# Performance work log

Measured on AMD Instinct MI355X. Metric: run time of the kernel, lower is better.

The kernel has to match this reference:

```python
import jax, jax.numpy as jnp
import numpy as np
import math

B, T, D, H = 2, 2048, 1024, 16
DH = D // H


def setup_inputs() -> dict:
    key = jax.random.key(0)
    k1, k2, k3 = jax.random.split(key, 3)
    scale_in = 1.0 / math.sqrt(D)
    x = jax.random.normal(k1, (B, T, D), dtype=jnp.float32)
    w_qkv = jax.random.normal(k2, (D, 3 * D), dtype=jnp.float32) * scale_in
    b_qkv = jnp.zeros((3 * D,), dtype=jnp.float32)
    w_out = jax.random.normal(k3, (D, D), dtype=jnp.float32) * scale_in
    b_out = jnp.zeros((D,), dtype=jnp.float32)
    return {"x": x, "w_qkv": w_qkv, "b_qkv": b_qkv, "w_out": w_out, "b_out": b_out}


def reference(x, w_qkv, b_qkv, w_out, b_out):
    # Fused QKV projection: [B,T,3D]
    qkv = x @ w_qkv + b_qkv
    q, k, v = jnp.split(qkv, 3, axis=-1)
    # [B,H,T,DH]
    q = q.reshape(B, T, H, DH).transpose(0, 2, 1, 3)
    k = k.reshape(B, T, H, DH).transpose(0, 2, 1, 3)
    v = v.reshape(B, T, H, DH).transpose(0, 2, 1, 3)
    # scores: [B,H,T,T]
    scores = jnp.einsum('bhqd,bhkd->bhqk', q, k) / math.sqrt(DH)
    causal_mask = jnp.tril(jnp.ones((T, T), dtype=bool))
    scores = jnp.where(causal_mask, scores, -1e10)
    attn = jax.nn.softmax(scores, axis=-1)
    out = jnp.einsum('bhqk,bhkd->bhqd', attn, v)
    out = out.transpose(0, 2, 1, 3).reshape(B, T, D)
    return out @ w_out + b_out
```

## Files before the change

### kernel.cpp

```cpp
#include <hip/hip_runtime.h>
#include <hip/hip_bf16.h>
#include <stdint.h>

#define Bsz  2
#define Tseq 2048
#define Dmod 1024
#define Hn   16
#define DHd  64

typedef short bf16x8 __attribute__((ext_vector_type(8)));
typedef float f32x4 __attribute__((ext_vector_type(4)));

__device__ __forceinline__ float bf2f(unsigned short u) {
  union { unsigned int i; float f; } v; v.i = ((unsigned int)u) << 16; return v.f;
}
__device__ __forceinline__ unsigned short f2bf(float f) {
  union { float f; unsigned int i; } v; v.f = f;
  unsigned int r = (v.i + 0x7fffu + ((v.i >> 16) & 1u)) >> 16;
  return (unsigned short)r;
}
__device__ __forceinline__ unsigned int pk_bf16(float a, float b) {
  union { __hip_bfloat162 h; unsigned int u; } u2;
  u2.h = __float22bfloat162_rn(make_float2(a, b));
  return u2.u;
}
__device__ __forceinline__ void gl_lds16(const unsigned short* g, unsigned short* l) {
  __builtin_amdgcn_global_load_lds(
      (const __attribute__((address_space(1))) void*)g,
      (__attribute__((address_space(3))) void*)l, 16, 0, 0);
}

__global__ __launch_bounds__(256) void prep(const float* __restrict__ x,
                                            const float* __restrict__ w_qkv,
                                            const float* __restrict__ w_out,
                                            unsigned short* __restrict__ xb,
                                            unsigned short* __restrict__ wqkvT,
                                            unsigned short* __restrict__ woutT) {
  __shared__ unsigned short tile[64][65];
  const int blk = blockIdx.x;
  if (blk < 2048) {
    int idx = blk * 2048 + threadIdx.x * 8;
    float4 a = *(const float4*)&x[idx];
    float4 b = *(const float4*)&x[idx + 4];
    unsigned short o[8];
    o[0] = f2bf(a.x); o[1] = f2bf(a.y); o[2] = f2bf(a.z); o[3] = f2bf(a.w);
    o[4] = f2bf(b.x); o[5] = f2bf(b.y); o[6] = f2bf(b.z); o[7] = f2bf(b.w);
    *(uint4*)&xb[idx] = *(const uint4*)o;
    return;
  }
  const float* in;
  unsigned short* out;
  int K = 1024, N, k0, n0;
  if (blk < 2048 + 768) {
    int t = blk - 2048;
    in = w_qkv; out = wqkvT; N = 3072;
    n0 = (t % 48) * 64; k0 = (t / 48) * 64;
  } else {
    int t = blk - 2816;
    in = w_out; out = woutT; N = 1024;
    n0 = (t % 16) * 64; k0 = (t / 16) * 64;
  }
  for (int i = threadIdx.x; i < 4096; i += 256) {
    int r = i >> 6, c = i & 63;
    tile[r][c] = f2bf(in[(size_t)(k0 + r) * N + n0 + c]);
  }
  __syncthreads();
  for (int i = threadIdx.x; i < 4096; i += 256) {
    int r = i >> 6, c = i & 63;
    out[(size_t)(n0 + r) * K + k0 + c] = tile[c][r];
  }
}

template<int NT>
__global__ __launch_bounds__(256) void gemm_bt(const unsigned short* __restrict__ A,
                                               const unsigned short* __restrict__ Bt,
                                               const float* __restrict__ bias,
                                               int M, int N, int K, int mode,
                                               float* __restrict__ outF,
                                               unsigned short* __restrict__ out0,
                                               unsigned short* __restrict__ out1,
                                               unsigned short* __restrict__ out2) {
  constexpr int JT = NT / 32;
  constexpr int BP = NT / 32;
  __shared__ unsigned short As[2][128 * 64];
  __shared__ unsigned short Bs[2][NT * 64];
  const int tid  = threadIdx.x;
  const int lane = tid & 63;
  const int w    = tid >> 6;
  const int m0   = blockIdx.x * 128;
  const int n0   = blockIdx.y * NT;
  const int wr   = (w >> 1) * 64;
  const int wc   = (w & 1) * (NT / 2);

  f32x4 acc[4][JT];
  for (int i = 0; i < 4; i++)
    for (int j = 0; j < JT; j++)
      for (int v = 0; v < 4; v++) acc[i][j][v] = 0.0f;

  const int l16 = lane & 15;
  const int g   = lane >> 4;
  const int sw  = l16 & 7;

  const int csw = (((lane & 7) ^ (lane >> 3)) & 7) * 8;
  const unsigned short* ga[4];
  const unsigned short* gb[BP];
  unsigned short* la[2][4];
  unsigned short* lb[2][BP];
#pragma unroll
  for (int p = 0; p < 4; p++) {
    int r = 32 * w + 8 * p + (lane >> 3);
    ga[p] = A + (size_t)(m0 + r) * K + csw;
    la[0][p] = &As[0][(32 * w + 8 * p) * 64];
    la[1][p] = &As[1][(32 * w + 8 * p) * 64];
  }
#pragma unroll
  for (int p = 0; p < BP; p++) {
    int r = (NT / 4) * w + 8 * p + (lane >> 3);
    gb[p] = Bt + (size_t)(n0 + r) * K + csw;
    lb[0][p] = &Bs[0][((NT / 4) * w + 8 * p) * 64];
    lb[1][p] = &Bs[1][((NT / 4) * w + 8 * p) * 64];
  }

#pragma unroll
  for (int p = 0; p < 4; p++) gl_lds16(ga[p], la[0][p]);
#pragma unroll
  for (int p = 0; p < BP; p++) gl_lds16(gb[p], lb[0][p]);
  __syncthreads();

  for (int kt = 0; kt < K; kt += 64) {
    const int cur = (kt >> 6) & 1, nxt = cur ^ 1;
    if (kt + 64 < K) {
#pragma unroll
      for (int p = 0; p < 4; p++) gl_lds16(ga[p] + kt + 64, la[nxt][p]);
#pragma unroll
      for (int p = 0; p < BP; p++) gl_lds16(gb[p] + kt + 64, lb[nxt][p]);
    }
#pragma unroll
    for (int ks = 0; ks < 2; ks++) {
      bf16x8 af[4], bf[JT];
#pragma unroll
      for (int i = 0; i < 4; i++)
        af[i] = *(const bf16x8*)&As[cur][(wr + i * 16 + l16) * 64 + (((ks * 4 + g) ^ sw) * 8)];
#pragma unroll
      for (int j = 0; j < JT; j++)
        bf[j] = *(const bf16x8*)&Bs[cur][(wc + j * 16 + l16) * 64 + (((ks * 4 + g) ^ sw) * 8)];
#pragma unroll
      for (int i = 0; i < 4; i++)
#pragma unroll
        for (int j = 0; j < JT; j++)
          acc[i][j] = __builtin_amdgcn_mfma_f32_16x16x32_bf16(af[i], bf[j], acc[i][j], 0, 0, 0);
    }
    __syncthreads();
  }

  const int q4 = g * 4;
#pragma unroll
  for (int i = 0; i < 4; i++)
#pragma unroll
    for (int j = 0; j < JT; j++) {
      const int mbase = m0 + wr + i * 16 + q4;
      const int n = n0 + wc + j * 16 + l16;
      float vals[4];
#pragma unroll
      for (int v = 0; v < 4; v++) vals[v] = acc[i][j][v] + bias[n];
      if (mode == 1) {
#pragma unroll
        for (int v = 0; v < 4; v++)
          outF[(size_t)(mbase + v) * N + n] = vals[v];
      } else {
        const int which = n >> 10;
        const int rem = n & 1023;
        const int h = rem >> 6, dd = rem & 63;
        const int b = mbase >> 11, t = mbase & 2047;
        if (which == 2) {
          uint2 uu;
          uu.x = pk_bf16(vals[0], vals[1]);
          uu.y = pk_bf16(vals[2], vals[3]);
          *(uint2*)&out2[((size_t)((b * Hn + h) * DHd + dd)) * Tseq + t] = uu;
        } else {
          unsigned short* dst = (which == 0) ? out0 : out1;
#pragma unroll
          for (int v = 0; v < 4; v++)
            dst[(size_t)((b * Hn + h) * Tseq + t + v) * DHd + dd] = f2bf(vals[v]);
        }
      }
    }
}

__global__ __launch_bounds__(256, 3) void attn_mfma(const unsigned short* __restrict__ Qb,
                                                    const unsigned short* __restrict__ Kb,
                                                    const unsigned short* __restrict__ Vtg,
                                                    unsigned short* __restrict__ O) {
  __shared__ unsigned short Ks[2][64 * 64];
  __shared__ unsigned short Vs[2][64 * 64];
  __shared__ unsigned short Ps[4][16 * 72];

  const int tid  = threadIdx.x;
  const int lane = tid & 63;
  const int w    = tid >> 6;
  const int g    = lane >> 4;
  const int l16  = lane & 15;
  const int bh   = blockIdx.x;
  const int tile = (int)gridDim.y - 1 - (int)blockIdx.y;
  const int q0w  = tile * 64 + w * 16;

  const unsigned short* Qp = Qb  + (size_t)bh * Tseq * DHd;
  const unsigned short* Kp = Kb  + (size_t)bh * Tseq * DHd;
  const unsigned short* Vp = Vtg + (size_t)bh * DHd * Tseq;

  bf16x8 qf[2];
#pragma unroll
  for (int ks = 0; ks < 2; ks++)
    qf[ks] = *(const bf16x8*)&Qp[(size_t)(q0w + l16) * DHd + ks * 32 + g * 8];

  f32x4 Oacc[4];
#pragma unroll
  for (int dt = 0; dt < 4; dt++)
#pragma unroll
    for (int v = 0; v < 4; v++) Oacc[dt][v] = 0.f;

  float mrow = -1e30f, lrow = 0.f;
  unsigned short* Pw = Ps[w];

  const int csw = (((lane & 7) ^ (lane >> 3)) & 7) * 8;
  const unsigned short* KgB = Kp + (size_t)(16 * w + (lane >> 3)) * DHd + csw;
  const unsigned short* VgB = Vp + (size_t)(16 * w + (lane >> 3)) * Tseq + csw;
  unsigned short* KsW[2] = { &Ks[0][16 * w * 64], &Ks[1][16 * w * 64] };
  unsigned short* VsW[2] = { &Vs[0][16 * w * 64], &Vs[1][16 * w * 64] };

  gl_lds16(KgB,             KsW[0]);
  gl_lds16(KgB + 8 * DHd,   KsW[0] + 8 * 64);
  gl_lds16(VgB,             VsW[0]);
  gl_lds16(VgB + 8 * Tseq,  VsW[0] + 8 * 64);
  __syncthreads();

  for (int c = 0; c <= tile; c++) {
    const int cur = c & 1, nxt = cur ^ 1;
    if (c < tile) {
      const size_t ko = (size_t)(c + 1) * 64 * DHd;
      const int    vo = (c + 1) * 64;
      gl_lds16(KgB + ko,            KsW[nxt]);
      gl_lds16(KgB + ko + 8 * DHd,  KsW[nxt] + 8 * 64);
      gl_lds16(VgB + vo,            VsW[nxt]);
      gl_lds16(VgB + vo + 8 * Tseq, VsW[nxt] + 8 * 64);
    }

    f32x4 st[4];
#pragma unroll
    for (int mt = 0; mt < 4; mt++)
#pragma unroll
      for (int v = 0; v < 4; v++) st[mt][v] = 0.f;
#pragma unroll
    for (int ks = 0; ks < 2; ks++) {
      bf16x8 kf[4];
#pragma unroll
      for (int mt = 0; mt < 4; mt++)
        kf[mt] = *(const bf16x8*)&Ks[cur][(16 * mt + l16) * 64 + (((ks * 4 + g) ^ (l16 & 7)) * 8)];
#pragma unroll
      for (int mt = 0; mt < 4; mt++)
        st[mt] = __builtin_amdgcn_mfma_f32_16x16x32_bf16(kf[mt], qf[ks], st[mt], 0, 0, 0);
    }

    const float SC = 0.1803368801f;
    float mx = -1e30f;
    if (c == tile) {
      const int qg = q0w + l16;
#pragma unroll
      for (int mt = 0; mt < 4; mt++)
#pragma unroll
        for (int v = 0; v < 4; v++) {
          float s = st[mt][v] * SC;
          if ((c * 64 + 16 * mt + 4 * g + v) > qg) s = -1e30f;
          st[mt][v] = s;
          mx = fmaxf(mx, s);
        }
    } else {
#pragma unroll
      for (int mt = 0; mt < 4; mt++)
#pragma unroll
        for (int v = 0; v < 4; v++) {
          float s = st[mt][v] * SC;
          st[mt][v] = s;
          mx = fmaxf(mx, s);
        }
    }
    mx = fmaxf(mx, __shfl_xor(mx, 16));
    mx = fmaxf(mx, __shfl_xor(mx, 32));
    const float mn = fmaxf(mrow, mx);
    const float alpha = __builtin_exp2f(mrow - mn);
    mrow = mn;
    float psum = 0.f;
#pragma unroll
    for (int mt = 0; mt < 4; mt++) {
      float p[4];
#pragma unroll
      for (int v = 0; v < 4; v++) { p[v] = __builtin_exp2f(st[mt][v] - mn); psum += p[v]; }
      uint2 uu;
      uu.x = pk_bf16(p[0], p[1]);
      uu.y = pk_bf16(p[2], p[3]);
      *(uint2*)&Pw[l16 * 72 + 16 * mt + 4 * g] = uu;
    }
    psum += __shfl_xor(psum, 16);
    psum += __shfl_xor(psum, 32);
    lrow = lrow * alpha + psum;

    const float a0 = __shfl(alpha, 4 * g + 0);
    const float a1 = __shfl(alpha, 4 * g + 1);
    const float a2 = __shfl(alpha, 4 * g + 2);
    const float a3 = __shfl(alpha, 4 * g + 3);
#pragma unroll
    for (int dt = 0; dt < 4; dt++) {
      Oacc[dt][0] *= a0;
      Oacc[dt][1] *= a1;
      Oacc[dt][2] *= a2;
      Oacc[dt][3] *= a3;
    }

#pragma unroll
    for (int ks = 0; ks < 2; ks++) {
      bf16x8 pf = *(const bf16x8*)&Pw[l16 * 72 + ks * 32 + g * 8];
      bf16x8 vf[4];
#pragma unroll
      for (int dt = 0; dt < 4; dt++)
        vf[dt] = *(const bf16x8*)&Vs[cur][(16 * dt + l16) * 64 + (((ks * 4 + g) ^ (l16 & 7)) * 8)];
#pragma unroll
      for (int dt = 0; dt < 4; dt++)
        Oacc[dt] = __builtin_amdgcn_mfma_f32_16x16x32_bf16(pf, vf[dt], Oacc[dt], 0, 0, 0);
    }

    __syncthreads();
  }

  const float l0 = __shfl(lrow, 4 * g + 0);
  const float l1 = __shfl(lrow, 4 * g + 1);
  const float l2 = __shfl(lrow, 4 * g + 2);
  const float l3 = __shfl(lrow, 4 * g + 3);
  const float i0 = 1.f / l0, i1 = 1.f / l1, i2 = 1.f / l2, i3 = 1.f / l3;
  const int b = bh >> 4, h = bh & 15;
#pragma unroll
  for (int dt = 0; dt < 4; dt++) {
    const int d = h * DHd + 16 * dt + l16;
    const size_t r0 = (size_t)(b * Tseq + q0w + 4 * g) * Dmod + d;
    O[r0]            = f2bf(Oacc[dt][0] * i0);
    O[r0 + Dmod]     = f2bf(Oacc[dt][1] * i1);
    O[r0 + 2 * Dmod] = f2bf(Oacc[dt][2] * i2);
    O[r0 + 3 * Dmod] = f2bf(Oacc[dt][3] * i3);
  }
}

extern "C" void kernel_launch(void* const* d_in, const int* in_sizes, int n_in,
                              void* d_out, int out_size, void* d_ws, size_t ws_size,
                              hipStream_t stream) {
  (void)in_sizes; (void)n_in; (void)out_size; (void)ws_size;
  const float* x     = (const float*)d_in[0];
  const float* w_qkv = (const float*)d_in[1];
  const float* b_qkv = (const float*)d_in[2];
  const float* w_out = (const float*)d_in[3];
  const float* b_out = (const float*)d_in[4];
  float* out = (float*)d_out;

  unsigned short* ws    = (unsigned short*)d_ws;
  unsigned short* xb    = ws;
  unsigned short* wqkvT = xb    + (size_t)4194304;
  unsigned short* woutT = wqkvT + (size_t)3072 * 1024;
  unsigned short* Qb    = woutT + (size_t)1024 * 1024;
  unsigned short* Kb    = Qb + (size_t)4194304;
  unsigned short* Vt    = Kb + (size_t)4194304;
  unsigned short* Ob    = xb;

  prep<<<3072, 256, 0, stream>>>(x, w_qkv, w_out, xb, wqkvT, woutT);
  gemm_bt<128><<<dim3(32, 24), 256, 0, stream>>>(xb, wqkvT, b_qkv, 4096, 3072, 1024, 0,
                                                 nullptr, Qb, Kb, Vt);
  attn_mfma<<<dim3(32, 32), 256, 0, stream>>>(Qb, Kb, Vt, Ob);
  gemm_bt<64><<<dim3(32, 16), 256, 0, stream>>>(Ob, woutT, b_out, 4096, 1024, 1024, 1,
                                                out, nullptr, nullptr, nullptr);
}
```

Measured before the change: 179.9 us.

## Enlarge attention query tile to 128 rows and fold softmax scale into Q

Each attention block now covers 128 query rows: every wave handles two 16-row query subtiles against each K/V chunk in LDS, which halves the grid and reuses each loaded K/V tile for twice as many queries. The softmax scale (including log2e) is applied to Q in the QKV GEMM epilogue, so the per-score multiply in the attention loop goes away. In exchange there is more register pressure (doubled accumulators and score tiles), fewer blocks to spread over the CUs, and some waves sit idle in the final causal chunk while still joining the barrier.

```diff
diff --git a/kernel.cpp b/kernel.cpp
--- a/kernel.cpp
+++ b/kernel.cpp
@@ -29,6 +29,8 @@
       (const __attribute__((address_space(1))) void*)g,
       (__attribute__((address_space(3))) void*)l, 16, 0, 0);
 }
+
+#define QSCALE 0.1803368801f
 
 __global__ __launch_bounds__(256) void prep(const float* __restrict__ x,
                                             const float* __restrict__ w_qkv,
@@ -177,11 +179,14 @@
           uu.x = pk_bf16(vals[0], vals[1]);
           uu.y = pk_bf16(vals[2], vals[3]);
           *(uint2*)&out2[((size_t)((b * Hn + h) * DHd + dd)) * Tseq + t] = uu;
+        } else if (which == 0) {
+#pragma unroll
+          for (int v = 0; v < 4; v++)
+            out0[(size_t)((b * Hn + h) * Tseq + t + v) * DHd + dd] = f2bf(vals[v] * QSCALE);
         } else {
-          unsigned short* dst = (which == 0) ? out0 : out1;
 #pragma unroll
           for (int v = 0; v < 4; v++)
-            dst[(size_t)((b * Hn + h) * Tseq + t + v) * DHd + dd] = f2bf(vals[v]);
+            out1[(size_t)((b * Hn + h) * Tseq + t + v) * DHd + dd] = f2bf(vals[v]);
         }
       }
     }
@@ -193,7 +198,7 @@
                                                     unsigned short* __restrict__ O) {
   __shared__ unsigned short Ks[2][64 * 64];
   __shared__ unsigned short Vs[2][64 * 64];
-  __shared__ unsigned short Ps[4][16 * 72];
+  __shared__ unsigned short Ps[4][32 * 72];
 
   const int tid  = threadIdx.x;
   const int lane = tid & 63;
@@ -202,24 +207,29 @@
   const int l16  = lane & 15;
   const int bh   = blockIdx.x;
   const int tile = (int)gridDim.y - 1 - (int)blockIdx.y;
-  const int q0w  = tile * 64 + w * 16;
+  const int q0w  = tile * 128 + w * 32;
 
   const unsigned short* Qp = Qb  + (size_t)bh * Tseq * DHd;
   const unsigned short* Kp = Kb  + (size_t)bh * Tseq * DHd;
   const unsigned short* Vp = Vtg + (size_t)bh * DHd * Tseq;
 
-  bf16x8 qf[2];
-#pragma unroll
-  for (int ks = 0; ks < 2; ks++)
-    qf[ks] = *(const bf16x8*)&Qp[(size_t)(q0w + l16) * DHd + ks * 32 + g * 8];
-
-  f32x4 Oacc[4];
-#pragma unroll
-  for (int dt = 0; dt < 4; dt++)
-#pragma unroll
-    for (int v = 0; v < 4; v++) Oacc[dt][v] = 0.f;
-
-  float mrow = -1e30f, lrow = 0.f;
+  bf16x8 qf[2][2];
+#pragma unroll
+  for (int qt = 0; qt < 2; qt++)
+#pragma unroll
+    for (int ks = 0; ks < 2; ks++)
+      qf[qt][ks] = *(const bf16x8*)&Qp[(size_t)(q0w + 16 * qt + l16) * DHd + ks * 32 + g * 8];
+
+  f32x4 Oacc[2][4];
+#pragma unroll
+  for (int qt = 0; qt < 2; qt++)
+#pragma unroll
+    for (int dt = 0; dt < 4; dt++)
+#pragma unroll
+      for (int v = 0; v < 4; v++) Oacc[qt][dt][v] = 0.f;
+
+  float mrow[2] = {-1e30f, -1e30f};
+  float lrow[2] = {0.f, 0.f};
   unsigned short* Pw = Ps[w];
 
   const int csw = (((lane & 7) ^ (lane >> 3)) & 7) * 8;
@@ -234,9 +244,11 @@
   gl_lds16(VgB + 8 * Tseq,  VsW[0] + 8 * 64);
   __syncthreads();
 
-  for (int c = 0; c <= tile; c++) {
+  const int cmax = (q0w + 31) >> 6;
+  const int nch  = 2 * tile + 2;
+  for (int c = 0; c < nch; c++) {
     const int cur = c & 1, nxt = cur ^ 1;
-    if (c < tile) {
+    if (c + 1 < nch) {
       const size_t ko = (size_t)(c + 1) * 64 * DHd;
       const int    vo = (c + 1) * 64;
       gl_lds16(KgB + ko,            KsW[nxt]);
@@ -245,106 +257,118 @@
       gl_lds16(VgB + vo + 8 * Tseq, VsW[nxt] + 8 * 64);
     }
 
-    f32x4 st[4];
-#pragma unroll
-    for (int mt = 0; mt < 4; mt++)
-#pragma unroll
-      for (int v = 0; v < 4; v++) st[mt][v] = 0.f;
-#pragma unroll
-    for (int ks = 0; ks < 2; ks++) {
-      bf16x8 kf[4];
+    if (c <= cmax) {
+      f32x4 st[4][2];
 #pragma unroll
       for (int mt = 0; mt < 4; mt++)
-        kf[mt] = *(const bf16x8*)&Ks[cur][(16 * mt + l16) * 64 + (((ks * 4 + g) ^ (l16 & 7)) * 8)];
-#pragma unroll
-      for (int mt = 0; mt < 4; mt++)
-        st[mt] = __builtin_amdgcn_mfma_f32_16x16x32_bf16(kf[mt], qf[ks], st[mt], 0, 0, 0);
-    }
-
-    const float SC = 0.1803368801f;
-    float mx = -1e30f;
-    if (c == tile) {
-      const int qg = q0w + l16;
-#pragma unroll
-      for (int mt = 0; mt < 4; mt++)
-#pragma unroll
-        for (int v = 0; v < 4; v++) {
-          float s = st[mt][v] * SC;
-          if ((c * 64 + 16 * mt + 4 * g + v) > qg) s = -1e30f;
-          st[mt][v] = s;
-          mx = fmaxf(mx, s);
+#pragma unroll
+        for (int qt = 0; qt < 2; qt++)
+#pragma unroll
+          for (int v = 0; v < 4; v++) st[mt][qt][v] = 0.f;
+#pragma unroll
+      for (int ks = 0; ks < 2; ks++) {
+        bf16x8 kf[4];
+#pragma unroll
+        for (int mt = 0; mt < 4; mt++)
+          kf[mt] = *(const bf16x8*)&Ks[cur][(16 * mt + l16) * 64 + (((ks * 4 + g) ^ (l16 & 7)) * 8)];
+#pragma unroll
+        for (int mt = 0; mt < 4; mt++)
+#pragma unroll
+          for (int qt = 0; qt < 2; qt++)
+            st[mt][qt] = __builtin_amdgcn_mfma_f32_16x16x32_bf16(kf[mt], qf[qt][ks], st[mt][qt], 0, 0, 0);
+      }
+
+      const bool dm = (c == cmax);
+#pragma unroll
+      for (int qt = 0; qt < 2; qt++) {
+        const int qg = q0w + 16 * qt + l16;
+        float mx = -1e30f;
+        if (dm) {
+#pragma unroll
+          for (int mt = 0; mt < 4; mt++)
+#pragma unroll
+            for (int v = 0; v < 4; v++) {
+              float s = st[mt][qt][v];
+              if ((c * 64 + 16 * mt + 4 * g + v) > qg) s = -1e30f;
+              st[mt][qt][v] = s;
+              mx = fmaxf(mx, s);
+            }
+        } else {
+#pragma unroll
+          for (int mt = 0; mt < 4; mt++)
+#pragma unroll
+            for (int v = 0; v < 4; v++) mx = fmaxf(mx, st[mt][qt][v]);
         }
-    } else {
-#pragma unroll
-      for (int mt = 0; mt < 4; mt++)
-#pragma unroll
-        for (int v = 0; v < 4; v++) {
-          float s = st[mt][v] * SC;
-          st[mt][v] = s;
-          mx = fmaxf(mx, s);
+        mx = fmaxf(mx, __shfl_xor(mx, 16));
+        mx = fmaxf(mx, __shfl_xor(mx, 32));
+        const float mn = fmaxf(mrow[qt], mx);
+        const float alpha = __builtin_exp2f(mrow[qt] - mn);
+        mrow[qt] = mn;
+        float psum = 0.f;
+#pragma unroll
+        for (int mt = 0; mt < 4; mt++) {
+          float p[4];
+#pragma unroll
+          for (int v = 0; v < 4; v++) { p[v] = __builtin_exp2f(st[mt][qt][v] - mn); psum += p[v]; }
+          uint2 uu;
+          uu.x = pk_bf16(p[0], p[1]);
+          uu.y = pk_bf16(p[2], p[3]);
+          *(uint2*)&Pw[(16 * qt + l16) * 72 + 16 * mt + 4 * g] = uu;
         }
-    }
-    mx = fmaxf(mx, __shfl_xor(mx, 16));
-    mx = fmaxf(mx, __shfl_xor(mx, 32));
-    const float mn = fmaxf(mrow, mx);
-    const float alpha = __builtin_exp2f(mrow - mn);
-    mrow = mn;
-    float psum = 0.f;
-#pragma unroll
-    for (int mt = 0; mt < 4; mt++) {
-      float p[4];
-#pragma unroll
-      for (int v = 0; v < 4; v++) { p[v] = __builtin_exp2f(st[mt][v] - mn); psum += p[v]; }
-      uint2 uu;
-      uu.x = pk_bf16(p[0], p[1]);
-      uu.y = pk_bf16(p[2], p[3]);
-      *(uint2*)&Pw[l16 * 72 + 16 * mt + 4 * g] = uu;
-    }
-    psum += __shfl_xor(psum, 16);
-    psum += __shfl_xor(psum, 32);
-    lrow = lrow * alpha + psum;
-
-    const float a0 = __shfl(alpha, 4 * g + 0);
-    const float a1 = __shfl(alpha, 4 * g + 1);
-    const float a2 = __shfl(alpha, 4 * g + 2);
-    const float a3 = __shfl(alpha, 4 * g + 3);
+        psum += __shfl_xor(psum, 16);
+        psum += __shfl_xor(psum, 32);
+        lrow[qt] = lrow[qt] * alpha + psum;
+
+        const float a0 = __shfl(alpha, 4 * g + 0);
+        const float a1 = __shfl(alpha, 4 * g + 1);
+        const float a2 = __shfl(alpha, 4 * g + 2);
+        const float a3 = __shfl(alpha, 4 * g + 3);
+#pragma unroll
+        for (int dt = 0; dt < 4; dt++) {
+          Oacc[qt][dt][0] *= a0;
+          Oacc[qt][dt][1] *= a1;
+          Oacc[qt][dt][2] *= a2;
+          Oacc[qt][dt][3] *= a3;
+        }
+      }
+
+#pragma unroll
+      for (int ks = 0; ks < 2; ks++) {
+        bf16x8 pf[2], vf[4];
+#pragma unroll
+        for (int qt = 0; qt < 2; qt++)
+          pf[qt] = *(const bf16x8*)&Pw[(16 * qt + l16) * 72 + ks * 32 + g * 8];
+#pragma unroll
+        for (int dt = 0; dt < 4; dt++)
+          vf[dt] = *(const bf16x8*)&Vs[cur][(16 * dt + l16) * 64 + (((ks * 4 + g) ^ (l16 & 7)) * 8)];
+#pragma unroll
+        for (int qt = 0; qt < 2; qt++)
+#pragma unroll
+          for (int dt = 0; dt < 4; dt++)
+            Oacc[qt][dt] = __builtin_amdgcn_mfma_f32_16x16x32_bf16(pf[qt], vf[dt], Oacc[qt][dt], 0, 0, 0);
+      }
+    }
+
+    __syncthreads();
+  }
+
+  const int b = bh >> 4, h = bh & 15;
+#pragma unroll
+  for (int qt = 0; qt < 2; qt++) {
+    const float l0 = __shfl(lrow[qt], 4 * g + 0);
+    const float l1 = __shfl(lrow[qt], 4 * g + 1);
+    const float l2 = __shfl(lrow[qt], 4 * g + 2);
+    const float l3 = __shfl(lrow[qt], 4 * g + 3);
+    const float i0 = 1.f / l0, i1 = 1.f / l1, i2 = 1.f / l2, i3 = 1.f / l3;
 #pragma unroll
     for (int dt = 0; dt < 4; dt++) {
-      Oacc[dt][0] *= a0;
-      Oacc[dt][1] *= a1;
-      Oacc[dt][2] *= a2;
-      Oacc[dt][3] *= a3;
-    }
-
-#pragma unroll
-    for (int ks = 0; ks < 2; ks++) {
-      bf16x8 pf = *(const bf16x8*)&Pw[l16 * 72 + ks * 32 + g * 8];
-      bf16x8 vf[4];
-#pragma unroll
-      for (int dt = 0; dt < 4; dt++)
-        vf[dt] = *(const bf16x8*)&Vs[cur][(16 * dt + l16) * 64 + (((ks * 4 + g) ^ (l16 & 7)) * 8)];
-#pragma unroll
-      for (int dt = 0; dt < 4; dt++)
-        Oacc[dt] = __builtin_amdgcn_mfma_f32_16x16x32_bf16(pf, vf[dt], Oacc[dt], 0, 0, 0);
-    }
-
-    __syncthreads();
-  }
-
-  const float l0 = __shfl(lrow, 4 * g + 0);
-  const float l1 = __shfl(lrow, 4 * g + 1);
-  const float l2 = __shfl(lrow, 4 * g + 2);
-  const float l3 = __shfl(lrow, 4 * g + 3);
-  const float i0 = 1.f / l0, i1 = 1.f / l1, i2 = 1.f / l2, i3 = 1.f / l3;
-  const int b = bh >> 4, h = bh & 15;
-#pragma unroll
-  for (int dt = 0; dt < 4; dt++) {
-    const int d = h * DHd + 16 * dt + l16;
-    const size_t r0 = (size_t)(b * Tseq + q0w + 4 * g) * Dmod + d;
-    O[r0]            = f2bf(Oacc[dt][0] * i0);
-    O[r0 + Dmod]     = f2bf(Oacc[dt][1] * i1);
-    O[r0 + 2 * Dmod] = f2bf(Oacc[dt][2] * i2);
-    O[r0 + 3 * Dmod] = f2bf(Oacc[dt][3] * i3);
+      const int d = h * DHd + 16 * dt + l16;
+      const size_t r0 = (size_t)(b * Tseq + q0w + 16 * qt + 4 * g) * Dmod + d;
+      O[r0]            = f2bf(Oacc[qt][dt][0] * i0);
+      O[r0 + Dmod]     = f2bf(Oacc[qt][dt][1] * i1);
+      O[r0 + 2 * Dmod] = f2bf(Oacc[qt][dt][2] * i2);
+      O[r0 + 3 * Dmod] = f2bf(Oacc[qt][dt][3] * i3);
+    }
   }
 }
 
@@ -371,7 +395,7 @@
   prep<<<3072, 256, 0, stream>>>(x, w_qkv, w_out, xb, wqkvT, woutT);
   gemm_bt<128><<<dim3(32, 24), 256, 0, stream>>>(xb, wqkvT, b_qkv, 4096, 3072, 1024, 0,
                                                  nullptr, Qb, Kb, Vt);
-  attn_mfma<<<dim3(32, 32), 256, 0, stream>>>(Qb, Kb, Vt, Ob);
+  attn_mfma<<<dim3(32, 16), 256, 0, stream>>>(Qb, Kb, Vt, Ob);
   gemm_bt<64><<<dim3(32, 16), 256, 0, stream>>>(Ob, woutT, b_out, 4096, 1024, 1024, 1,
                                                 out, nullptr, nullptr, nullptr);
 }
```

Result: slower. 201.7 us (+12.1%).
